# Kernel optimization log

Measured on AMD Instinct MI355X. Metric: run time of the kernel, lower is better.

## Reference

```python
import jax, jax.numpy as jnp
import numpy as np

T = 4096      # tokens (flattened batch*seq)
DIN = 2048    # input hidden dim
DQ = 2048     # q output dim
DKV = 2048    # per-head-group kv output dim (== DQ here, MHA)
NA = 4        # number of adapters (LoRA/delta models)
R = 16        # lora rank per q/k/v


def setup_inputs() -> dict:
    key = jax.random.key(0)
    ks = jax.random.split(key, 8)
    def rn(k, shape, scale):
        return jax.random.normal(k, shape, dtype=jnp.float32) * scale
    return {
        "x": rn(ks[0], (T, DIN), 1.0),
        "W_base": rn(ks[1], (DQ + 2 * DKV, DIN), DIN ** -0.5),
        "A_buffer_qkv": rn(ks[2], (NA, DIN, 3 * R), DIN ** -0.5),
        "B_buffer_q": rn(ks[3], (NA, R, DQ), R ** -0.5),
        "B_buffer_kv": rn(ks[4], (NA, R, 2 * DKV), R ** -0.5),
        "DeltaW_q": rn(ks[5], (NA, DIN, DQ), DIN ** -0.5),
        "DeltaW_kv": rn(ks[6], (NA, DIN, 2 * DKV), DIN ** -0.5),
        "weight_indices": jax.random.randint(ks[7], (T,), 0, NA, dtype=jnp.int32),
    }


def _ldmm(indices, x, A, B, D):
    """Per-token adapter-indexed (LoRA + dense delta) matmul.
    indices: [T] int, x: [T, din], A: [na, din, r], B: [na, r, dout], D: [na, din, dout].
    out[t] = (x[t] @ A[a]) @ B[a] + x[t] @ D[a]  with a = indices[t].
    Implemented as masked GEMMs over the small fixed adapter set.
    """
    na = A.shape[0]
    out = jnp.zeros((x.shape[0], B.shape[2]), dtype=x.dtype)
    for a in range(na):  # small fixed loop over adapters
        xa = jnp.where((indices == a)[:, None], x, jnp.zeros((), x.dtype))
        out = out + (xa @ A[a]) @ B[a] + xa @ D[a]
    return out


def reference(x, W_base, A_buffer_qkv, B_buffer_q, B_buffer_kv,
              DeltaW_q, DeltaW_kv, weight_indices):
    # base QKV projection (ColumnParallelLinear, no bias): [T, dq + 2*dkv]
    base = x @ W_base.T
    rank = A_buffer_qkv.shape[2] // 3
    b_dim_q = B_buffer_q.shape[2]
    b_dim_kv = B_buffer_kv.shape[2] // 2
    d_dim_kv = DeltaW_kv.shape[2] // 2
    for i in range(3):  # q, k, v slices
        if i == 0:
            o = _ldmm(weight_indices, x,
                      A_buffer_qkv[:, :, :rank], B_buffer_q, DeltaW_q)
            base = base.at[:, :b_dim_q].add(o)
        else:
            o = _ldmm(weight_indices, x,
                      A_buffer_qkv[:, :, i * rank:(i + 1) * rank],
                      B_buffer_kv[:, :, (i - 1) * b_dim_kv:i * b_dim_kv],
                      DeltaW_kv[:, :, (i - 1) * d_dim_kv:i * d_dim_kv])
            base = base.at[:, i * b_dim_kv:(i + 1) * b_dim_kv].add(o)
    return base
```

## Files before the change

### kernel.cpp

```cpp
#include <hip/hip_runtime.h>
#include <stdint.h>

#define T_TOK 4096
#define DIN   2048
#define DQ    2048
#define DKV   2048
#define NOUT  (DQ + 2*DKV)
#define NA    4
#define RLORA 16
#define BM    256
#define BN    256
#define MPAD  (T_TOK + NA*BM)
#define MTILES (MPAD/BM)
#define KX    (DIN + 64)
#define NT    (KX/64)
#define KSPLIT 16
#define NTBLK (NOUT/BN)
#define NWG   (MTILES*NTBLK)

typedef unsigned short u16;
typedef __attribute__((ext_vector_type(8))) short short8;
typedef __attribute__((ext_vector_type(8))) u16 u16x8;
typedef __attribute__((ext_vector_type(4))) float f32x4;

__device__ __forceinline__ u16 f2bf(float f) {
  uint32_t u = __float_as_uint(f);
  u = (u + 0x7FFFu + ((u >> 16) & 1u)) >> 16;
  return (u16)u;
}
__device__ __forceinline__ float bf2f(u16 u) {
  return __uint_as_float(((uint32_t)u) << 16);
}

typedef __attribute__((address_space(3))) void lds_void;
typedef __attribute__((address_space(1))) void glb_void;

__device__ __forceinline__ void gl_lds16(const void* g, void* l) {
  __builtin_amdgcn_global_load_lds((const glb_void*)(uintptr_t)g,
                                   (lds_void*)(uint32_t)(uintptr_t)l, 16, 0, 0);
}

__global__ void prep_kernel(const int* __restrict__ widx,
                            int* __restrict__ tok,
                            int* __restrict__ tileAdapter) {
  __shared__ int cnt[256][NA];
  __shared__ int total[NA];
  __shared__ int pad_off[NA];
  const int tid = threadIdx.x;
  const int CH = T_TOK / 256;
  const int base = tid * CH;
  int c[NA] = {0, 0, 0, 0};
  for (int i = 0; i < CH; i++) c[widx[base + i]]++;
  for (int a = 0; a < NA; a++) cnt[tid][a] = c[a];
  __syncthreads();
  if (tid < NA) {
    int s = 0;
    for (int i = 0; i < 256; i++) { int v = cnt[i][tid]; cnt[i][tid] = s; s += v; }
    total[tid] = s;
  }
  __syncthreads();
  if (tid == 0) {
    int off = 0;
    for (int a = 0; a < NA; a++) {
      pad_off[a] = off;
      int ntile = (total[a] + BM - 1) / BM;
      for (int tl = 0; tl < ntile; tl++) tileAdapter[off / BM + tl] = a;
      off += ntile * BM;
    }
    for (int tl = off / BM; tl < MTILES; tl++) tileAdapter[tl] = -1;
  }
  __syncthreads();
  for (int i = tid; i < MPAD; i += 256) tok[i] = -1;
  __syncthreads();
  int myoff[NA];
  for (int a = 0; a < NA; a++) myoff[a] = pad_off[a] + cnt[tid][a];
  for (int i = 0; i < CH; i++) {
    int a = widx[base + i];
    tok[myoff[a]++] = base + i;
  }
}

__global__ void gather_kernel(const float* __restrict__ x,
                              const int* __restrict__ tok,
                              u16* __restrict__ Xg) {
  const int row = blockIdx.x;
  const int t = tok[row];
  const int tid = threadIdx.x;
  u16x8* dst = (u16x8*)(Xg + (size_t)row * KX);
  if (t < 0) {
    u16x8 z = {0, 0, 0, 0, 0, 0, 0, 0};
    dst[tid] = z;
    return;
  }
  const f32x4* src = (const f32x4*)(x + (size_t)t * DIN);
  f32x4 v0 = src[tid * 2];
  f32x4 v1 = src[tid * 2 + 1];
  u16x8 o;
  o[0] = f2bf(v0[0]); o[1] = f2bf(v0[1]); o[2] = f2bf(v0[2]); o[3] = f2bf(v0[3]);
  o[4] = f2bf(v1[0]); o[5] = f2bf(v1[1]); o[6] = f2bf(v1[2]); o[7] = f2bf(v1[3]);
  dst[tid] = o;
}

__global__ __launch_bounds__(256) void xa_partial_kernel(
    const u16* __restrict__ Xg, const float* __restrict__ A_qkv,
    const int* __restrict__ tileAdapter, float* __restrict__ Ppart) {
  const int ks = blockIdx.y;
  const int ad = tileAdapter[blockIdx.x >> 1];
  const int a = ad < 0 ? 0 : ad;
  const int kb = ks * (DIN / KSPLIT);
  const int tid = threadIdx.x;
  const int rg = tid >> 2;
  const int jg = tid & 3;
  const int r0 = blockIdx.x * 128 + rg * 2;
  const int j0 = jg * 12;
  __shared__ float ldsA[64][56];
  float acc[2][12];
  #pragma unroll
  for (int r = 0; r < 2; r++)
    #pragma unroll
    for (int j = 0; j < 12; j++) acc[r][j] = 0.f;

  for (int kc = 0; kc < 2; kc++) {
    const int kbase = kb + kc * 64;
    for (int i = tid; i < 64 * 48; i += 256) {
      int kk = i / 48, j = i - kk * 48;
      ldsA[kk][j] = A_qkv[((size_t)a * DIN + kbase + kk) * (3 * RLORA) + j];
    }
    __syncthreads();
    u16x8 xr[2][8];
    #pragma unroll
    for (int r = 0; r < 2; r++)
      #pragma unroll
      for (int q = 0; q < 8; q++)
        xr[r][q] = *(const u16x8*)(Xg + (size_t)(r0 + r) * KX + kbase + q * 8);
    #pragma unroll
    for (int q = 0; q < 8; q++) {
      #pragma unroll
      for (int e = 0; e < 8; e++) {
        const int kk = q * 8 + e;
        f32x4 a0 = *(const f32x4*)&ldsA[kk][j0];
        f32x4 a1 = *(const f32x4*)&ldsA[kk][j0 + 4];
        f32x4 a2 = *(const f32x4*)&ldsA[kk][j0 + 8];
        float x0 = bf2f(xr[0][q][e]);
        float x1 = bf2f(xr[1][q][e]);
        #pragma unroll
        for (int c = 0; c < 4; c++) {
          acc[0][c]     += x0 * a0[c];  acc[1][c]     += x1 * a0[c];
          acc[0][4 + c] += x0 * a1[c];  acc[1][4 + c] += x1 * a1[c];
          acc[0][8 + c] += x0 * a2[c];  acc[1][8 + c] += x1 * a2[c];
        }
      }
    }
    __syncthreads();
  }
  #pragma unroll
  for (int r = 0; r < 2; r++)
    #pragma unroll
    for (int j = 0; j < 12; j++)
      Ppart[((size_t)ks * MPAD + r0 + r) * 48 + j0 + j] = acc[r][j];
}

__global__ void xa_reduce_kernel(const float* __restrict__ Ppart,
                                 u16* __restrict__ Xg) {
  const int gid = blockIdx.x * 256 + threadIdx.x;
  const int row = gid >> 6, j = gid & 63;
  float s = 0.f;
  if (j < 48) {
    #pragma unroll
    for (int sp = 0; sp < KSPLIT; sp++)
      s += Ppart[((size_t)sp * MPAD + row) * 48 + j];
  }
  Xg[(size_t)row * KX + DIN + j] = f2bf(s);
}

__global__ __launch_bounds__(256) void weff2_kernel(
    const float* __restrict__ W_base,
    const float* __restrict__ DW_q, const float* __restrict__ DW_kv,
    u16* __restrict__ Weff) {
  const int k0 = blockIdx.x * 64;
  const int n0 = blockIdx.y * 64;
  const int tid = threadIdx.x;
  const int k8 = (tid & 7) * 8;
  __shared__ float ldsD[64][65];

  f32x4 wb[2][2];
  #pragma unroll
  for (int h = 0; h < 2; h++) {
    const int nn = h * 32 + (tid >> 3);
    const float* p = W_base + (size_t)(n0 + nn) * DIN + k0 + k8;
    wb[h][0] = *(const f32x4*)p;
    wb[h][1] = *(const f32x4*)(p + 4);
  }

  const int ldD  = (n0 < DQ) ? DQ : 2 * DKV;
  const int ncol = (n0 < DQ) ? n0 : n0 - DQ;

  for (int a = 0; a < NA; a++) {
    const float* Dp = (n0 < DQ)
        ? DW_q  + (size_t)a * DIN * DQ + ncol
        : DW_kv + (size_t)a * DIN * (2 * DKV) + ncol;
    for (int i = tid; i < 64 * 64; i += 256) {
      int kk = i >> 6, nn2 = i & 63;
      ldsD[kk][nn2] = Dp[(size_t)(k0 + kk) * ldD + nn2];
    }
    __syncthreads();
    #pragma unroll
    for (int h = 0; h < 2; h++) {
      const int nn = h * 32 + (tid >> 3);
      u16x8 o;
      #pragma unroll
      for (int j = 0; j < 8; j++)
        o[j] = f2bf(wb[h][j >> 2][j & 3] + ldsD[k8 + j][nn]);
      *(u16x8*)(Weff + ((size_t)a * NOUT + n0 + nn) * KX + k0 + k8) = o;
    }
    __syncthreads();
  }
}

__global__ void wslots_kernel(const float* __restrict__ B_q,
                              const float* __restrict__ B_kv,
                              u16* __restrict__ Weff) {
  const int a = blockIdx.y;
  const int n = blockIdx.x * 256 + threadIdx.x;
  const int seg = n >> 11;
  u16 vals[64];
  #pragma unroll
  for (int j = 0; j < 64; j++) vals[j] = 0;
  if (seg == 0) {
    const float* Bp = B_q + ((size_t)a * RLORA) * DQ + n;
    for (int r = 0; r < RLORA; r++) vals[r] = f2bf(Bp[(size_t)r * DQ]);
  } else {
    const float* Bp = B_kv + ((size_t)a * RLORA) * (2 * DKV) + (n - DQ);
    for (int r = 0; r < RLORA; r++)
      vals[seg * RLORA + r] = f2bf(Bp[(size_t)r * (2 * DKV)]);
  }
  u16* dst = Weff + ((size_t)a * NOUT + n) * KX + DIN;
  #pragma unroll
  for (int v = 0; v < 8; v++) *(u16x8*)(dst + v * 8) = *(u16x8*)(vals + v * 8);
}

#define BAR    asm volatile("s_barrier" ::: "memory")
#define WAITV0 asm volatile("s_waitcnt vmcnt(0)" ::: "memory")

#define DSREAD(base, row, cb) \
  (*(const short8*)((const char*)(base) + ((row) * 128 + (cb))))

#define LOAD_A(Al, mh) { \
  _Pragma("unroll") for (int mi2 = 0; mi2 < 4; ++mi2) { \
    const int ar = wm * 128 + ((mh) * 4 + mi2) * 16 + fr; \
    af[mi2][0] = DSREAD(Al, ar, ksl ^ sw); \
    af[mi2][1] = DSREAD(Al, ar, (64 + ksl) ^ sw); \
  } }

#define LOAD_B(Bl, nh) { \
  _Pragma("unroll") for (int ni2 = 0; ni2 < 2; ++ni2) { \
    const int br = wn * 64 + ((nh) * 2 + ni2) * 16 + fr; \
    bf[ni2][0] = DSREAD(Bl, br, ksl ^ sw); \
    bf[ni2][1] = DSREAD(Bl, br, (64 + ksl) ^ sw); \
  } }

#define MFMA16(mh, nh) { \
  __builtin_amdgcn_s_setprio(1); \
  _Pragma("unroll") for (int mi2 = 0; mi2 < 4; ++mi2) \
  _Pragma("unroll") for (int ni2 = 0; ni2 < 2; ++ni2) { \
    acc[(mh)*4+mi2][(nh)*2+ni2] = __builtin_amdgcn_mfma_f32_16x16x32_bf16( \
        af[mi2][0], bf[ni2][0], acc[(mh)*4+mi2][(nh)*2+ni2], 0, 0, 0); \
    acc[(mh)*4+mi2][(nh)*2+ni2] = __builtin_amdgcn_mfma_f32_16x16x32_bf16( \
        af[mi2][1], bf[ni2][1], acc[(mh)*4+mi2][(nh)*2+ni2], 0, 0, 0); \
  } \
  __builtin_amdgcn_s_setprio(0); }

#define STAGE_T(ldsbase, gptr, ktE) { \
  _Pragma("unroll") for (int j = 0; j < 4; ++j) \
    gl_lds16((gptr) + (size_t)(j * 64) * KX + (ktE), \
             (u16*)(ldsbase) + (size_t)(j * 512 + tid) * 8); }

__global__ __launch_bounds__(512, 2) void gemm256_kernel(
    const u16* __restrict__ Xg, const u16* __restrict__ Weff,
    const int* __restrict__ tok, const int* __restrict__ tileAdapter,
    float* __restrict__ out) {
  __shared__ __align__(16) u16 As[2][256 * 64];
  __shared__ __align__(16) u16 Bs[2][256 * 64];

  const int bid = blockIdx.x;
  const int wg = (bid & 7) * (NWG / 8) + (bid >> 3);
  const int mt = wg % MTILES, nt = wg / MTILES;
  const int a = tileAdapter[mt];
  if (a < 0) return;
  const int m0 = mt * BM, n0 = nt * BN;
  const u16* Ag = Xg + (size_t)m0 * KX;
  const u16* Bg = Weff + (size_t)a * NOUT * KX + (size_t)n0 * KX;

  const int tid = threadIdx.x;
  const int l = tid & 63, w = tid >> 6;
  const int wm = w >> 2, wn = w & 3;

  const int fr = l & 15;
  const int ksl = (l >> 4) << 4;
  const int sw = (l & 7) << 4;

  const int srow = tid >> 3;
  const int scol = (((tid & 7) * 16) ^ ((srow & 7) << 4)) >> 1;
  const u16* gAs = Ag + (size_t)srow * KX + scol;
  const u16* gBs = Bg + (size_t)srow * KX + scol;

  u16* const A0w = &As[0][0];  u16* const A1w = &As[1][0];
  u16* const B0w = &Bs[0][0];  u16* const B1w = &Bs[1][0];
  const u16* const A0r = A0w;  const u16* const A1r = A1w;
  const u16* const B0r = B0w;  const u16* const B1r = B1w;

  f32x4 acc[8][4];
  #pragma unroll
  for (int i = 0; i < 8; i++)
    #pragma unroll
    for (int j = 0; j < 4; j++) acc[i][j] = (f32x4){0.f, 0.f, 0.f, 0.f};

  short8 af[4][2], bf[2][2];

  STAGE_T(A0w, gAs, 0);
  STAGE_T(B0w, gBs, 0);
  WAITV0;
  BAR;

  for (int pair = 0; pair < NT / 2; ++pair) {
    const int ktA = (2 * pair + 1) * 64;
    const int ktB = (2 * pair + 2) * 64;
    LOAD_A(A0r, 0); LOAD_B(B0r, 0); STAGE_T(A1w, gAs, ktA); BAR; MFMA16(0, 0); BAR;
    LOAD_B(B0r, 1);                 STAGE_T(B1w, gBs, ktA); BAR; MFMA16(0, 1); BAR;
    LOAD_A(A0r, 1); LOAD_B(B0r, 0);                         BAR; MFMA16(1, 0); BAR;
    LOAD_B(B0r, 1);                                         BAR; MFMA16(1, 1);
    WAITV0; BAR;
    LOAD_A(A1r, 0); LOAD_B(B1r, 0); STAGE_T(A0w, gAs, ktB); BAR; MFMA16(0, 0); BAR;
    LOAD_B(B1r, 1);                 STAGE_T(B0w, gBs, ktB); BAR; MFMA16(0, 1); BAR;
    LOAD_A(A1r, 1); LOAD_B(B1r, 0);                         BAR; MFMA16(1, 0); BAR;
    LOAD_B(B1r, 1);                                         BAR; MFMA16(1, 1);
    WAITV0; BAR;
  }
  LOAD_A(A0r, 0); LOAD_B(B0r, 0); BAR; MFMA16(0, 0); BAR;
  LOAD_B(B0r, 1);                 BAR; MFMA16(0, 1); BAR;
  LOAD_A(A0r, 1); LOAD_B(B0r, 0); BAR; MFMA16(1, 0); BAR;
  LOAD_B(B0r, 1);                 BAR; MFMA16(1, 1);

  #pragma unroll
  for (int mi = 0; mi < 8; ++mi) {
    const int rb = m0 + wm * 128 + mi * 16 + ((l >> 4) << 2);
    int tt[4];
    #pragma unroll
    for (int reg = 0; reg < 4; ++reg) tt[reg] = tok[rb + reg];
    #pragma unroll
    for (int ni = 0; ni < 4; ++ni) {
      const int col = n0 + wn * 64 + ni * 16 + fr;
      #pragma unroll
      for (int reg = 0; reg < 4; ++reg)
        if (tt[reg] >= 0) out[(size_t)tt[reg] * NOUT + col] = acc[mi][ni][reg];
    }
  }
}

__global__ void fallback_kernel(const float* __restrict__ x,
                                const float* __restrict__ W_base,
                                const float* __restrict__ A_qkv,
                                const float* __restrict__ B_q,
                                const float* __restrict__ B_kv,
                                const float* __restrict__ DW_q,
                                const float* __restrict__ DW_kv,
                                const int* __restrict__ widx,
                                float* __restrict__ out) {
  const int t = blockIdx.x;
  const int n = blockIdx.y * 256 + threadIdx.x;
  const int a = widx[t];
  __shared__ float xs[DIN];
  __shared__ float ys[3 * RLORA];
  for (int k = threadIdx.x; k < DIN; k += 256) xs[k] = x[(size_t)t * DIN + k];
  __syncthreads();
  if (threadIdx.x < 3 * RLORA) {
    float s = 0.f;
    const float* Ap = A_qkv + (size_t)a * DIN * (3 * RLORA) + threadIdx.x;
    for (int k = 0; k < DIN; k++) s += xs[k] * Ap[(size_t)k * (3 * RLORA)];
    ys[threadIdx.x] = s;
  }
  __syncthreads();
  const float* dcol; int ldD, roff; const float* bcol; int ldB;
  if (n < DQ) {
    dcol = DW_q + (size_t)a * DIN * DQ + n; ldD = DQ; roff = 0;
    bcol = B_q + (size_t)a * RLORA * DQ + n; ldB = DQ;
  } else {
    dcol = DW_kv + (size_t)a * DIN * (2 * DKV) + (n - DQ); ldD = 2 * DKV;
    roff = (n < 2 * DQ) ? RLORA : 2 * RLORA;
    bcol = B_kv + (size_t)a * RLORA * (2 * DKV) + (n - DQ); ldB = 2 * DKV;
  }
  const float* wrow = W_base + (size_t)n * DIN;
  float acc = 0.f;
  for (int k = 0; k < DIN; k++) acc += xs[k] * (wrow[k] + dcol[(size_t)k * ldD]);
  for (int r = 0; r < RLORA; r++) acc += ys[roff + r] * bcol[(size_t)r * ldB];
  out[(size_t)t * NOUT + n] = acc;
}

extern "C" void kernel_launch(void* const* d_in, const int* in_sizes, int n_in,
                              void* d_out, int out_size, void* d_ws, size_t ws_size,
                              hipStream_t stream) {
  const float* x      = (const float*)d_in[0];
  const float* W_base = (const float*)d_in[1];
  const float* A_qkv  = (const float*)d_in[2];
  const float* B_q    = (const float*)d_in[3];
  const float* B_kv   = (const float*)d_in[4];
  const float* DW_q   = (const float*)d_in[5];
  const float* DW_kv  = (const float*)d_in[6];
  const int*   widx   = (const int*)d_in[7];
  float* out = (float*)d_out;

  const size_t WEFF_BYTES = (size_t)NA * NOUT * KX * sizeof(u16);
  const size_t XG_BYTES   = (size_t)MPAD * KX * sizeof(u16);
  const size_t TOK_BYTES  = (size_t)MPAD * sizeof(int);
  const size_t TILE_BYTES = (size_t)MTILES * sizeof(int);
  const size_t need = WEFF_BYTES + XG_BYTES + TOK_BYTES + TILE_BYTES;

  if (ws_size < need) {
    fallback_kernel<<<dim3(T_TOK, NOUT / 256), 256, 0, stream>>>(
        x, W_base, A_qkv, B_q, B_kv, DW_q, DW_kv, widx, out);
    return;
  }

  char* ws = (char*)d_ws;
  u16* Weff = (u16*)ws;
  u16* Xg   = (u16*)(ws + WEFF_BYTES);
  int* tok  = (int*)(ws + WEFF_BYTES + XG_BYTES);
  int* tileAdapter = tok + MPAD;
  float* Ppart = (float*)ws;

  prep_kernel<<<1, 256, 0, stream>>>(widx, tok, tileAdapter);
  gather_kernel<<<MPAD, 256, 0, stream>>>(x, tok, Xg);
  xa_partial_kernel<<<dim3(MPAD / 128, KSPLIT), 256, 0, stream>>>(
      Xg, A_qkv, tileAdapter, Ppart);
  xa_reduce_kernel<<<MPAD * 64 / 256, 256, 0, stream>>>(Ppart, Xg);
  weff2_kernel<<<dim3(DIN / 64, NOUT / 64), 256, 0, stream>>>(
      W_base, DW_q, DW_kv, Weff);
  wslots_kernel<<<dim3(NOUT / 256, NA), 256, 0, stream>>>(B_q, B_kv, Weff);
  gemm256_kernel<<<dim3(NWG), 512, 0, stream>>>(
      Xg, Weff, tok, tileAdapter, out);
}
```

Before: 266.6 us.

## Replace double-buffered 64-K GEMM loop with 4-stage 32-K async pipeline

After: 262.8 us. About the same (-1.4%).

```diff
diff --git a/kernel.cpp b/kernel.cpp
--- a/kernel.cpp
+++ b/kernel.cpp
@@ -13,7 +13,7 @@
 #define MPAD  (T_TOK + NA*BM)
 #define MTILES (MPAD/BM)
 #define KX    (DIN + 64)
-#define NT    (KX/64)
+#define NKT   (KX/32)
 #define KSPLIT 16
 #define NTBLK (NOUT/BN)
 #define NWG   (MTILES*NTBLK)
@@ -228,59 +228,57 @@
   for (int j = 0; j < 64; j++) vals[j] = 0;
   if (seg == 0) {
     const float* Bp = B_q + ((size_t)a * RLORA) * DQ + n;
+    #pragma unroll
     for (int r = 0; r < RLORA; r++) vals[r] = f2bf(Bp[(size_t)r * DQ]);
+  } else if (seg == 1) {
+    const float* Bp = B_kv + ((size_t)a * RLORA) * (2 * DKV) + (n - DQ);
+    #pragma unroll
+    for (int r = 0; r < RLORA; r++) vals[RLORA + r] = f2bf(Bp[(size_t)r * (2 * DKV)]);
   } else {
     const float* Bp = B_kv + ((size_t)a * RLORA) * (2 * DKV) + (n - DQ);
-    for (int r = 0; r < RLORA; r++)
-      vals[seg * RLORA + r] = f2bf(Bp[(size_t)r * (2 * DKV)]);
+    #pragma unroll
+    for (int r = 0; r < RLORA; r++) vals[2 * RLORA + r] = f2bf(Bp[(size_t)r * (2 * DKV)]);
   }
   u16* dst = Weff + ((size_t)a * NOUT + n) * KX + DIN;
   #pragma unroll
   for (int v = 0; v < 8; v++) *(u16x8*)(dst + v * 8) = *(u16x8*)(vals + v * 8);
 }
 
-#define BAR    asm volatile("s_barrier" ::: "memory")
-#define WAITV0 asm volatile("s_waitcnt vmcnt(0)" ::: "memory")
-
-#define DSREAD(base, row, cb) \
-  (*(const short8*)((const char*)(base) + ((row) * 128 + (cb))))
-
-#define LOAD_A(Al, mh) { \
-  _Pragma("unroll") for (int mi2 = 0; mi2 < 4; ++mi2) { \
-    const int ar = wm * 128 + ((mh) * 4 + mi2) * 16 + fr; \
-    af[mi2][0] = DSREAD(Al, ar, ksl ^ sw); \
-    af[mi2][1] = DSREAD(Al, ar, (64 + ksl) ^ sw); \
-  } }
-
-#define LOAD_B(Bl, nh) { \
-  _Pragma("unroll") for (int ni2 = 0; ni2 < 2; ++ni2) { \
-    const int br = wn * 64 + ((nh) * 2 + ni2) * 16 + fr; \
-    bf[ni2][0] = DSREAD(Bl, br, ksl ^ sw); \
-    bf[ni2][1] = DSREAD(Bl, br, (64 + ksl) ^ sw); \
-  } }
-
-#define MFMA16(mh, nh) { \
+#define BAR      asm volatile("s_barrier" ::: "memory")
+#define WAITV(n) asm volatile("s_waitcnt vmcnt(" #n ")" ::: "memory")
+
+#define STAGE(b, t) { \
+  const u16* gA_ = gAs + (size_t)(t) * 32; \
+  const u16* gB_ = gBs + (size_t)(t) * 32; \
+  u16* lA_ = &lds[b][0][0] + tid * 8; \
+  u16* lB_ = &lds[b][1][0] + tid * 8; \
+  gl_lds16(gA_, lA_); \
+  gl_lds16(gA_ + (size_t)128 * KX, lA_ + 4096); \
+  gl_lds16(gB_, lB_); \
+  gl_lds16(gB_ + (size_t)128 * KX, lB_ + 4096); \
+}
+
+#define COMPUTE(b) { \
+  const char* Ab = (const char*)&lds[b][0][0]; \
+  const char* Bb = (const char*)&lds[b][1][0]; \
+  short8 af[8], bfr[4]; \
+  _Pragma("unroll") for (int mi = 0; mi < 8; ++mi) \
+    af[mi] = *(const short8*)(Ab + (wm * 128 + mi * 16) * 64 + laneoff); \
+  _Pragma("unroll") for (int ni = 0; ni < 4; ++ni) \
+    bfr[ni] = *(const short8*)(Bb + (wn * 64 + ni * 16) * 64 + laneoff); \
   __builtin_amdgcn_s_setprio(1); \
-  _Pragma("unroll") for (int mi2 = 0; mi2 < 4; ++mi2) \
-  _Pragma("unroll") for (int ni2 = 0; ni2 < 2; ++ni2) { \
-    acc[(mh)*4+mi2][(nh)*2+ni2] = __builtin_amdgcn_mfma_f32_16x16x32_bf16( \
-        af[mi2][0], bf[ni2][0], acc[(mh)*4+mi2][(nh)*2+ni2], 0, 0, 0); \
-    acc[(mh)*4+mi2][(nh)*2+ni2] = __builtin_amdgcn_mfma_f32_16x16x32_bf16( \
-        af[mi2][1], bf[ni2][1], acc[(mh)*4+mi2][(nh)*2+ni2], 0, 0, 0); \
-  } \
-  __builtin_amdgcn_s_setprio(0); }
-
-#define STAGE_T(ldsbase, gptr, ktE) { \
-  _Pragma("unroll") for (int j = 0; j < 4; ++j) \
-    gl_lds16((gptr) + (size_t)(j * 64) * KX + (ktE), \
-             (u16*)(ldsbase) + (size_t)(j * 512 + tid) * 8); }
+  _Pragma("unroll") for (int mi = 0; mi < 8; ++mi) \
+  _Pragma("unroll") for (int ni = 0; ni < 4; ++ni) \
+    acc[mi][ni] = __builtin_amdgcn_mfma_f32_16x16x32_bf16( \
+        af[mi], bfr[ni], acc[mi][ni], 0, 0, 0); \
+  __builtin_amdgcn_s_setprio(0); \
+}
 
 __global__ __launch_bounds__(512, 2) void gemm256_kernel(
     const u16* __restrict__ Xg, const u16* __restrict__ Weff,
     const int* __restrict__ tok, const int* __restrict__ tileAdapter,
     float* __restrict__ out) {
-  __shared__ __align__(16) u16 As[2][256 * 64];
-  __shared__ __align__(16) u16 Bs[2][256 * 64];
+  __shared__ __align__(16) u16 lds[4][2][256 * 32];
 
   const int bid = blockIdx.x;
   const int wg = (bid & 7) * (NWG / 8) + (bid >> 3);
@@ -288,26 +286,17 @@
   const int a = tileAdapter[mt];
   if (a < 0) return;
   const int m0 = mt * BM, n0 = nt * BN;
-  const u16* Ag = Xg + (size_t)m0 * KX;
-  const u16* Bg = Weff + (size_t)a * NOUT * KX + (size_t)n0 * KX;
 
   const int tid = threadIdx.x;
   const int l = tid & 63, w = tid >> 6;
   const int wm = w >> 2, wn = w & 3;
-
   const int fr = l & 15;
-  const int ksl = (l >> 4) << 4;
-  const int sw = (l & 7) << 4;
-
-  const int srow = tid >> 3;
-  const int scol = (((tid & 7) * 16) ^ ((srow & 7) << 4)) >> 1;
-  const u16* gAs = Ag + (size_t)srow * KX + scol;
-  const u16* gBs = Bg + (size_t)srow * KX + scol;
-
-  u16* const A0w = &As[0][0];  u16* const A1w = &As[1][0];
-  u16* const B0w = &Bs[0][0];  u16* const B1w = &Bs[1][0];
-  const u16* const A0r = A0w;  const u16* const A1r = A1w;
-  const u16* const B0r = B0w;  const u16* const B1r = B1w;
+  const int laneoff = fr * 64 + ((((l >> 4) ^ ((fr >> 1) & 3))) << 4);
+
+  const int srow = tid >> 2;
+  const int scol = (((tid & 3) ^ ((tid >> 3) & 3))) * 8;
+  const u16* gAs = Xg + (size_t)(m0 + srow) * KX + scol;
+  const u16* gBs = Weff + ((size_t)a * NOUT + n0 + srow) * KX + scol;
 
   f32x4 acc[8][4];
   #pragma unroll
@@ -315,31 +304,19 @@
     #pragma unroll
     for (int j = 0; j < 4; j++) acc[i][j] = (f32x4){0.f, 0.f, 0.f, 0.f};
 
-  short8 af[4][2], bf[2][2];
-
-  STAGE_T(A0w, gAs, 0);
-  STAGE_T(B0w, gBs, 0);
-  WAITV0;
-  BAR;
-
-  for (int pair = 0; pair < NT / 2; ++pair) {
-    const int ktA = (2 * pair + 1) * 64;
-    const int ktB = (2 * pair + 2) * 64;
-    LOAD_A(A0r, 0); LOAD_B(B0r, 0); STAGE_T(A1w, gAs, ktA); BAR; MFMA16(0, 0); BAR;
-    LOAD_B(B0r, 1);                 STAGE_T(B1w, gBs, ktA); BAR; MFMA16(0, 1); BAR;
-    LOAD_A(A0r, 1); LOAD_B(B0r, 0);                         BAR; MFMA16(1, 0); BAR;
-    LOAD_B(B0r, 1);                                         BAR; MFMA16(1, 1);
-    WAITV0; BAR;
-    LOAD_A(A1r, 0); LOAD_B(B1r, 0); STAGE_T(A0w, gAs, ktB); BAR; MFMA16(0, 0); BAR;
-    LOAD_B(B1r, 1);                 STAGE_T(B0w, gBs, ktB); BAR; MFMA16(0, 1); BAR;
-    LOAD_A(A1r, 1); LOAD_B(B1r, 0);                         BAR; MFMA16(1, 0); BAR;
-    LOAD_B(B1r, 1);                                         BAR; MFMA16(1, 1);
-    WAITV0; BAR;
-  }
-  LOAD_A(A0r, 0); LOAD_B(B0r, 0); BAR; MFMA16(0, 0); BAR;
-  LOAD_B(B0r, 1);                 BAR; MFMA16(0, 1); BAR;
-  LOAD_A(A0r, 1); LOAD_B(B0r, 0); BAR; MFMA16(1, 0); BAR;
-  LOAD_B(B0r, 1);                 BAR; MFMA16(1, 1);
+  STAGE(0, 0);
+  STAGE(1, 1);
+  STAGE(2, 2);
+
+  for (int i = 0; i < NKT - 3; ++i) {
+    WAITV(8);
+    BAR;
+    STAGE((i + 3) & 3, i + 3);
+    COMPUTE(i & 3);
+  }
+  WAITV(8); BAR; COMPUTE((NKT - 3) & 3);
+  WAITV(4); BAR; COMPUTE((NKT - 2) & 3);
+  WAITV(0); BAR; COMPUTE((NKT - 1) & 3);
 
   #pragma unroll
   for (int mi = 0; mi < 8; ++mi) {
```
